# Kernel tuning notes

Measured on AMD Instinct MI355X. Metric: run time of the kernel, lower is better.

## Reference

```python
import jax, jax.numpy as jnp
import numpy as np

N = 40000          # nodes per type (dev, repo)
H, D = 8, 64       # heads, head dim
HID = H * D        # 512 hidden channels
OUT = 256
N_CONVS = 4        # 2 towers (res, link) x 2 layers
EDGE_TYPES = [(0, 1), (1, 0), (0, 0)]  # (src_type, dst_type)
SQRT_D = float(np.sqrt(D))


def _lin(x, w, b):
    return x @ w + b


def _seg_softmax(a, idx, n):
    m = jax.ops.segment_max(a, idx, num_segments=n)
    e = jnp.exp(a - m[idx])
    s = jax.ops.segment_sum(e, idx, num_segments=n)
    return e / (s[idx] + 1e-16)


def _hgt_conv(xs, edges, kw, kb, qw, qb, vw, vb, aw, ab, skip, a_rel, m_rel, p_rel):
    # xs: [x_dev, x_repo] each [N, HID]; edges: list of [2, E]
    k = [_lin(xs[t], kw[t], kb[t]).reshape(-1, H, D) for t in range(2)]
    q = [_lin(xs[t], qw[t], qb[t]).reshape(-1, H, D) for t in range(2)]
    v = [_lin(xs[t], vw[t], vb[t]).reshape(-1, H, D) for t in range(2)]
    out = [jnp.zeros_like(k[0]), jnp.zeros_like(k[1])]
    for r, (st, dt) in enumerate(EDGE_TYPES):
        src, dst = edges[r][0], edges[r][1]
        k_rel = jnp.einsum('nhd,hde->nhe', k[st], a_rel[r])
        v_rel = jnp.einsum('nhd,hde->nhe', v[st], m_rel[r])
        alpha = (q[dt][dst] * k_rel[src]).sum(-1) * p_rel[r] / SQRT_D  # [E, H]
        alpha = _seg_softmax(alpha, dst, N)
        msg = v_rel[src] * alpha[..., None]                            # [E, H, D]
        out[dt] = out[dt] + jax.ops.segment_sum(msg, dst, num_segments=N)
    res = []
    for t in range(2):
        o = _lin(jax.nn.gelu(out[t].reshape(-1, HID), approximate=False), aw[t], ab[t])
        g = jax.nn.sigmoid(skip[t])
        res.append(g * o + (1.0 - g) * xs[t])
    return res


def setup_inputs() -> dict:
    key = jax.random.key(0)
    ks = iter(jax.random.split(key, 48))
    def nrm(shape, scale=1.0):
        return jax.random.normal(next(ks), shape, dtype=jnp.float32) * scale
    E1, E2, E3, EP = 250000, 250000, 150000, 100000
    inp = {}
    inp['x_dev'] = nrm((N, HID))
    inp['x_repo'] = nrm((N, HID))
    inp['ei_dr'] = jax.random.randint(next(ks), (2, E1), 0, N, dtype=jnp.int32)
    inp['ei_rd'] = jax.random.randint(next(ks), (2, E2), 0, N, dtype=jnp.int32)
    inp['ei_dd'] = jax.random.randint(next(ks), (2, E3), 0, N, dtype=jnp.int32)
    inp['pos_edge'] = jax.random.randint(next(ks), (2, EP), 0, N, dtype=jnp.int32)
    inp['neg_edge'] = jax.random.randint(next(ks), (2, EP), 0, N, dtype=jnp.int32)
    s = 1.0 / np.sqrt(HID)
    for nm in ('k', 'q', 'v', 'a'):
        inp[nm + '_w'] = nrm((N_CONVS, 2, HID, HID), s)
        inp[nm + '_b'] = jnp.zeros((N_CONVS, 2, HID), jnp.float32)
    inp['skip'] = jnp.ones((N_CONVS, 2), jnp.float32)
    sd = 1.0 / np.sqrt(D)
    inp['a_rel'] = nrm((N_CONVS, 3, H, D, D), sd)
    inp['m_rel'] = nrm((N_CONVS, 3, H, D, D), sd)
    inp['p_rel'] = jnp.ones((N_CONVS, 3, H), jnp.float32)
    inp['reg_w1'] = nrm((HID, OUT), s); inp['reg_b1'] = jnp.zeros((OUT,), jnp.float32)
    inp['reg_w2'] = nrm((OUT, 1), 1.0 / np.sqrt(OUT)); inp['reg_b2'] = jnp.zeros((1,), jnp.float32)
    inp['src_w'] = nrm((HID, OUT), s); inp['src_b'] = jnp.zeros((OUT,), jnp.float32)
    inp['dst_w'] = nrm((HID, OUT), s); inp['dst_b'] = jnp.zeros((OUT,), jnp.float32)
    inp['fin_w'] = nrm((OUT, 1), 1.0 / np.sqrt(OUT)); inp['fin_b'] = jnp.zeros((1,), jnp.float32)
    return inp


def reference(x_dev, x_repo, ei_dr, ei_rd, ei_dd, pos_edge, neg_edge,
              k_w, k_b, q_w, q_b, v_w, v_b, a_w, a_b, skip,
              a_rel, m_rel, p_rel,
              reg_w1, reg_b1, reg_w2, reg_b2,
              src_w, src_b, dst_w, dst_b, fin_w, fin_b):
    edges = [ei_dr, ei_rd, ei_dd]

    def embed(conv_ids):
        xs = [x_dev, x_repo]
        for c in conv_ids:
            xs = _hgt_conv(xs, edges, k_w[c], k_b[c], q_w[c], q_b[c], v_w[c], v_b[c],
                           a_w[c], a_b[c], skip[c], a_rel[c], m_rel[c], p_rel[c])
            xs = [jax.nn.leaky_relu(x, 0.01) for x in xs]
        return xs

    res = embed([0, 1])   # embedding_res tower
    lnk = embed([2, 3])   # embedding_link tower
    emb_dev = res[0] + lnk[0]
    emb_repo = res[1] + lnk[1]

    fit_dev = _lin(_lin(emb_dev, reg_w1, reg_b1), reg_w2, reg_b2).squeeze(-1)
    fit_repo = _lin(_lin(emb_repo, reg_w1, reg_b1), reg_w2, reg_b2).squeeze(-1)

    def link(zs, zd):
        h = _lin(zs, src_w, src_b) * _lin(zd, dst_w, dst_b)
        return jax.nn.sigmoid(_lin(h, fin_w, fin_b)).squeeze(-1)

    pos = link(emb_dev[pos_edge[0]], emb_repo[pos_edge[1]])
    neg = link(emb_dev[neg_edge[0]], emb_repo[neg_edge[1]])
    score = jnp.concatenate([pos, neg], axis=0)
    return (fit_dev, fit_repo, score)
```

## Files before the change

kernel.cpp:

```cpp
#include <hip/hip_runtime.h>
#include <math.h>

#define NNODES 40000
#define NB ((size_t)20480000)
#define RPS 40004

typedef __attribute__((ext_vector_type(8))) short bf16x8;
typedef __attribute__((ext_vector_type(4))) float f32x4;

__device__ __forceinline__ ushort f2bf(float f) {
  unsigned u = __float_as_uint(f);
  u += 0x7FFFu + ((u >> 16) & 1u);
  return (ushort)(u >> 16);
}
__device__ __forceinline__ float b2f(ushort h) {
  return __uint_as_float((unsigned)h << 16);
}
__device__ __forceinline__ float gelu_f(float x) {
  return 0.5f * x * (1.0f + erff(x * 0.70710678118654752440f));
}

__device__ __forceinline__ void gll16(const ushort* g, ushort* l) {
  __builtin_amdgcn_global_load_lds(
      (const __attribute__((address_space(1))) unsigned int*)(const void*)g,
      (__attribute__((address_space(3))) unsigned int*)(void*)l, 16, 0, 0);
}

template<int EPI>
__global__ __launch_bounds__(256)
void gemm_bf16_kernel(const ushort* __restrict__ Av, const ushort* __restrict__ Bt,
                      const float* __restrict__ bias,
                      ushort* __restrict__ C0, ushort* __restrict__ C1,
                      int M, int PW, int RS,
                      const ushort* __restrict__ xprev, const float* __restrict__ skipv,
                      int nwgx)
{
  const int K = 512;
  __shared__ char smem[32768];
  ushort* Sm = (ushort*)smem;
  float*  Es = (float*)smem;

  const int nwg = (int)gridDim.x;
  const int q8 = nwg >> 3, r8 = nwg & 7;
  const int xcd = (int)blockIdx.x & 7, i8 = (int)blockIdx.x >> 3;
  const int logical = (xcd < r8 ? xcd * (q8 + 1) : r8 * (q8 + 1) + (xcd - r8) * q8) + i8;
  const int bm = (logical / nwgx) * 128;
  const int bnl = (logical % nwgx) * 128;
  const int pan = (bnl >= PW) ? 1 : 0;
  const int bn = bnl - pan * PW;
  ushort* __restrict__ C = pan ? C1 : C0;

  const int tid = threadIdx.x, lane = tid & 63, wave = tid >> 6;
  const int wr = (wave >> 1) * 64, wc = (wave & 1) * 64;
  const int fr = lane & 15, fq = lane >> 4;
  f32x4 acc[4][4] = {};

  const int rdsw = (fq ^ ((fr >> 1) & 3)) * 8;
  const int csrc = ((lane & 3) ^ ((lane >> 3) & 3)) * 8;
  const int r0 = wave * 32 + (lane >> 2);
  int ra0 = bm + r0;      if (ra0 >= M) ra0 = M - 1;
  int ra1 = bm + r0 + 16; if (ra1 >= M) ra1 = M - 1;
  const ushort* ga0 = Av + (size_t)ra0 * K + csrc;
  const ushort* ga1 = Av + (size_t)ra1 * K + csrc;
  const ushort* gb0 = Bt + (size_t)(bnl + r0) * K + csrc;
  const ushort* gb1 = Bt + (size_t)(bnl + r0 + 16) * K + csrc;
  ushort* la0[2] = {Sm + wave * 1024,        Sm + 8192 + wave * 1024};
  ushort* la1[2] = {la0[0] + 512,            la0[1] + 512};
  ushort* lb0[2] = {Sm + 4096 + wave * 1024, Sm + 12288 + wave * 1024};
  ushort* lb1[2] = {lb0[0] + 512,            lb0[1] + 512};

  gll16(ga0, la0[0]); gll16(ga1, la1[0]); gll16(gb0, lb0[0]); gll16(gb1, lb1[0]);
  ga0 += 32; ga1 += 32; gb0 += 32; gb1 += 32;
  gll16(ga0, la0[1]); gll16(ga1, la1[1]); gll16(gb0, lb0[1]); gll16(gb1, lb1[1]);
  ga0 += 32; ga1 += 32; gb0 += 32; gb1 += 32;

  #pragma unroll
  for (int it = 0; it < 16; ++it) {
    const int cur = it & 1;
    if (it < 15) asm volatile("s_waitcnt vmcnt(4)" ::: "memory");
    else         asm volatile("s_waitcnt vmcnt(0)" ::: "memory");
    __builtin_amdgcn_s_barrier();
    const ushort* Ab = Sm + cur * 8192;
    const ushort* Bb = Ab + 4096;
    bf16x8 af[4], bfv[4];
    #pragma unroll
    for (int i = 0; i < 4; ++i) {
      af[i]  = *(const bf16x8*)&Ab[(wr + i * 16 + fr) * 32 + rdsw];
      bfv[i] = *(const bf16x8*)&Bb[(wc + i * 16 + fr) * 32 + rdsw];
    }
    asm volatile("s_waitcnt lgkmcnt(0)" ::: "memory");
    __builtin_amdgcn_s_barrier();
    if (it < 14) {
      gll16(ga0, la0[cur]); gll16(ga1, la1[cur]); gll16(gb0, lb0[cur]); gll16(gb1, lb1[cur]);
      ga0 += 32; ga1 += 32; gb0 += 32; gb1 += 32;
    }
    #pragma unroll
    for (int mi = 0; mi < 4; ++mi)
      #pragma unroll
      for (int ni = 0; ni < 4; ++ni)
        acc[mi][ni] = __builtin_amdgcn_mfma_f32_16x16x32_bf16(af[mi], bfv[ni], acc[mi][ni], 0, 0, 0);
  }
  __syncthreads();

  float gate = 0.f, og = 0.f;
  if (EPI == 2) { gate = 1.f / (1.f + __expf(-skipv[0])); og = 1.f - gate; }
  #pragma unroll
  for (int qr = 0; qr < 4; ++qr) {
    __syncthreads();
    #pragma unroll
    for (int mi = 0; mi < 4; ++mi) {
      if (((wr + mi * 16) >> 5) != qr) continue;
      const int lr = ((wr + mi * 16) & 31) + fq * 4;
      #pragma unroll
      for (int ni = 0; ni < 4; ++ni) {
        const int col = wc + ni * 16 + fr;
        #pragma unroll
        for (int r = 0; r < 4; ++r)
          Es[(lr + r) * 132 + col] = acc[mi][ni][r];
      }
    }
    __syncthreads();
    const int lrow = tid >> 3;
    const int c0 = (tid & 7) * 16;
    const int grow = bm + qr * 32 + lrow;
    if (grow < M) {
      float v[16];
      #pragma unroll
      for (int j = 0; j < 4; ++j)
        *(float4*)&v[j * 4] = *(const float4*)&Es[lrow * 132 + c0 + j * 4];
      if (EPI == 1 || EPI == 2) {
        #pragma unroll
        for (int j = 0; j < 4; ++j) {
          float4 b4 = *(const float4*)(bias + bnl + c0 + j * 4);
          v[j*4] += b4.x; v[j*4+1] += b4.y; v[j*4+2] += b4.z; v[j*4+3] += b4.w;
        }
      }
      size_t base = (size_t)grow * RS + bn + c0;
      if (EPI == 2) {
        uint4 x0 = *(const uint4*)(xprev + base);
        uint4 x1 = *(const uint4*)(xprev + base + 8);
        #pragma unroll
        for (int j = 0; j < 8; ++j) {
          unsigned w = (j < 4) ? ((const unsigned*)&x0)[j] : ((const unsigned*)&x1)[j - 4];
          float a  = gate * v[2*j]   + og * __uint_as_float(w << 16);
          float bq = gate * v[2*j+1] + og * __uint_as_float(w & 0xFFFF0000u);
          v[2*j]   = a  > 0.f ? a  : 0.01f * a;
          v[2*j+1] = bq > 0.f ? bq : 0.01f * bq;
        }
      }
      if (EPI == 4) {
        uint4 x0 = *(const uint4*)(C + base);
        uint4 x1 = *(const uint4*)(C + base + 8);
        #pragma unroll
        for (int j = 0; j < 8; ++j) {
          unsigned w = (j < 4) ? ((const unsigned*)&x0)[j] : ((const unsigned*)&x1)[j - 4];
          v[2*j]   += __uint_as_float(w << 16);
          v[2*j+1] += __uint_as_float(w & 0xFFFF0000u);
        }
      }
      ushort ob[16];
      #pragma unroll
      for (int j = 0; j < 16; ++j) ob[j] = f2bf(v[j]);
      *(uint4*)(C + base)     = *(uint4*)&ob[0];
      *(uint4*)(C + base + 8) = *(uint4*)&ob[8];
    }
  }
}

__global__ __launch_bounds__(256)
void transpose_w_batch(const float* __restrict__ q_w, const float* __restrict__ a_w,
                       const float* __restrict__ src_w, const float* __restrict__ dst_w,
                       ushort* __restrict__ wqT, ushort* __restrict__ waT,
                       ushort* __restrict__ srcwT, ushort* __restrict__ dstwT)
{
  const int z = blockIdx.z;
  const float* W; ushort* Wt; int N;
  if (z < 8)       { W = q_w + (size_t)z * 262144;       Wt = wqT + (size_t)z * 262144;       N = 512; }
  else if (z < 16) { W = a_w + (size_t)(z - 8) * 262144; Wt = waT + (size_t)(z - 8) * 262144; N = 512; }
  else if (z == 16){ W = src_w; Wt = srcwT; N = 256; }
  else             { W = dst_w; Wt = dstwT; N = 256; }
  int bn = blockIdx.x * 32, bk = blockIdx.y * 32;
  if (bn >= N) return;
  __shared__ float t[32][33];
  int x = threadIdx.x & 31, y = threadIdx.x >> 5;
  #pragma unroll
  for (int yy = y; yy < 32; yy += 8) t[yy][x] = W[(size_t)(bk + yy) * N + bn + x];
  __syncthreads();
  #pragma unroll
  for (int yy = y; yy < 32; yy += 8) Wt[(size_t)(bn + yy) * 512 + bk + x] = f2bf(t[x][yy]);
}

__global__ __launch_bounds__(256)
void fold_rel_batch(const float* __restrict__ k_w, const float* __restrict__ k_b,
                    const float* __restrict__ v_w, const float* __restrict__ v_b,
                    const float* __restrict__ a_rel, const float* __restrict__ m_rel,
                    ushort* __restrict__ wkvT, float* __restrict__ bfuse)
{
  const int z = blockIdx.z;
  const int kv = z / 12, i = z % 12;
  const int c = i / 3, r = i % 3;
  const int st_tab[3] = {0, 1, 0};
  const int stp = st_tab[r];
  const float* Win  = (kv ? v_w : k_w) + (size_t)(c * 2 + stp) * 262144;
  const float* bin  = (kv ? v_b : k_b) + (size_t)(c * 2 + stp) * 512;
  const float* Arel = (kv ? m_rel : a_rel) + (size_t)i * 32768;
  const int h = blockIdx.x, kc = blockIdx.y;
  ushort* W2t = wkvT + (size_t)i * 524288 + (size_t)(h >> 2) * 262144
              + (size_t)(kv * 256 + (h & 3) * 64) * 512;
  float*  b2  = bfuse + i * 1024 + (h >> 2) * 512 + kv * 256 + (h & 3) * 64;

  __shared__ float Wl[64][65];
  __shared__ float Al[4096];
  for (int j = threadIdx.x; j < 4096; j += 256) Al[j] = Arel[(size_t)h * 4096 + j];
  {
    const int kk = threadIdx.x >> 2, d0 = (threadIdx.x & 3) * 16;
    const float* src = Win + (size_t)(kc * 64 + kk) * 512 + h * 64 + d0;
    #pragma unroll
    for (int j = 0; j < 4; ++j)
      *(float4*)&Wl[kk][d0 + j * 4] = *(const float4*)(src + j * 4);
  }
  __syncthreads();
  const int wave = threadIdx.x >> 6, lane = threadIdx.x & 63;
  #pragma unroll 4
  for (int rr = 0; rr < 16; ++rr) {
    const int e = wave * 16 + rr;
    float acc = 0.f;
    #pragma unroll
    for (int d = 0; d < 64; ++d) acc = fmaf(Wl[lane][d], Al[d * 64 + e], acc);
    W2t[(size_t)e * 512 + kc * 64 + lane] = f2bf(acc);
  }
  if (kc == 0 && wave == 0) {
    float acc = 0.f;
    #pragma unroll
    for (int d = 0; d < 64; ++d) acc = fmaf(bin[h * 64 + d], Al[d * 64 + lane], acc);
    b2[lane] = acc;
  }
}

__global__ __launch_bounds__(256)
void make_wfit_kernel(const float* __restrict__ w1, const float* __restrict__ b1,
                      const float* __restrict__ w2, const float* __restrict__ b2,
                      float* __restrict__ wfit)
{
  for (int k = threadIdx.x; k < 512; k += 256) {
    float acc = 0.f;
    for (int j = 0; j < 256; ++j) acc = fmaf(w1[(size_t)k * 256 + j], w2[j], acc);
    wfit[k] = acc;
  }
  if (threadIdx.x == 0) {
    float acc = 0.f;
    for (int j = 0; j < 256; ++j) acc = fmaf(b1[j], w2[j], acc);
    wfit[512] = acc + b2[0];
  }
}

__global__ __launch_bounds__(256)
void hist_batch(const int* __restrict__ d0, const int* __restrict__ d1,
                const int* __restrict__ d2, unsigned* __restrict__ cnt3)
{
  const int z = blockIdx.z;
  const int* dst = (z == 0) ? d0 : (z == 1) ? d1 : d2;
  const int E = (z == 2) ? 150000 : 250000;
  unsigned* cnt = cnt3 + (size_t)z * NNODES;
  for (int i = blockIdx.x * 256 + threadIdx.x; i < E; i += gridDim.x * 256)
    atomicAdd(&cnt[dst[i]], 1u);
}

__global__ __launch_bounds__(256)
void scan_batch(const unsigned* __restrict__ cnt3, unsigned* __restrict__ rowptr3,
                unsigned* __restrict__ woff3)
{
  const int z = blockIdx.x;
  const unsigned* cnt = cnt3 + (size_t)z * NNODES;
  unsigned* rowptr = rowptr3 + (size_t)z * RPS;
  unsigned* woff   = woff3 + (size_t)z * NNODES;
  __shared__ unsigned csum[256];
  const int t = threadIdx.x;
  const int lo = t * 160, hi = (lo + 160 < NNODES) ? lo + 160 : NNODES;
  unsigned s = 0;
  for (int i = lo; i < hi; i += 4) {
    uint4 v = *(const uint4*)&cnt[i];
    s += v.x + v.y + v.z + v.w;
  }
  csum[t] = s;
  __syncthreads();
  if (t == 0) {
    unsigned run = 0;
    for (int j = 0; j < 256; ++j) { unsigned v = csum[j]; csum[j] = run; run += v; }
    rowptr[NNODES] = run;
  }
  __syncthreads();
  unsigned run = csum[t];
  for (int i = lo; i < hi; i += 4) {
    uint4 cv = *(const uint4*)&cnt[i];
    uint4 rp;
    rp.x = run; run += cv.x;
    rp.y = run; run += cv.y;
    rp.z = run; run += cv.z;
    rp.w = run; run += cv.w;
    *(uint4*)&rowptr[i] = rp;
    *(uint4*)&woff[i]   = rp;
  }
}

__global__ __launch_bounds__(256)
void fill_batch(const int* __restrict__ e0, const int* __restrict__ e1,
                const int* __restrict__ e2, unsigned* __restrict__ woff3,
                unsigned* __restrict__ srcord)
{
  const int z = blockIdx.z;
  const int* e = (z == 0) ? e0 : (z == 1) ? e1 : e2;
  const int E = (z == 2) ? 150000 : 250000;
  const int* src = e;
  const int* dst = e + E;
  unsigned* woff = woff3 + (size_t)z * NNODES;
  unsigned* ord  = srcord + ((z == 0) ? 0 : (z == 1) ? 250000 : 500000);
  for (int i = blockIdx.x * 256 + threadIdx.x; i < E; i += gridDim.x * 256) {
    unsigned slot = atomicAdd(&woff[dst[i]], 1u);
    ord[slot] = (unsigned)src[i];
  }
}

template<int ACCUM, int GELU>
__global__ __launch_bounds__(256)
void fused_edge_kernel(const ushort* __restrict__ q, const ushort* __restrict__ KVh,
                      const unsigned* __restrict__ rowptr, const unsigned* __restrict__ srcord,
                      const float* __restrict__ prel, int hs,
                      const ushort* __restrict__ accin, ushort* __restrict__ outp)
{
  int d = (int)((blockIdx.x * 256u + threadIdx.x) >> 6);
  int lane = threadIdx.x & 63;
  if (d >= NNODES) return;
  unsigned start = rowptr[d], end = rowptr[d + 1];
  const int hl = lane >> 4;
  const int off = hl * 64 + (lane & 15) * 4;
  const float pscale = prel[hs * 4 + hl] * 0.125f;
  const size_t obase = (size_t)d * 512 + hs * 256 + off;

  uint2 qv = *(const uint2*)(q + obase);
  float qf0 = __uint_as_float(qv.x << 16),         qf1 = __uint_as_float(qv.x & 0xFFFF0000u);
  float qf2 = __uint_as_float(qv.y << 16),         qf3 = __uint_as_float(qv.y & 0xFFFF0000u);

  float m = -3e38f, ssum = 0.f;
  float a0 = 0.f, a1 = 0.f, a2 = 0.f, a3 = 0.f;
  if (start < end) {
    int sn = (int)srcord[start];
    const ushort* r0 = KVh + (size_t)sn * 512 + off;
    uint2 kv_c = *(const uint2*)r0;
    uint2 vv_c = *(const uint2*)(r0 + 256);
    const unsigned last = end - 1;
    for (unsigned idx = start; idx < end; ++idx) {
      unsigned idxn = (idx < last) ? idx + 1 : last;
      int sn2 = (int)srcord[idxn];
      const ushort* rn = KVh + (size_t)sn2 * 512 + off;
      uint2 kv_n = *(const uint2*)rn;
      uint2 vv_n = *(const uint2*)(rn + 256);
      float dot =      qf0 * __uint_as_float(kv_c.x << 16);
      dot = fmaf(qf1, __uint_as_float(kv_c.x & 0xFFFF0000u), dot);
      dot = fmaf(qf2, __uint_as_float(kv_c.y << 16),         dot);
      dot = fmaf(qf3, __uint_as_float(kv_c.y & 0xFFFF0000u), dot);
      dot += __shfl_xor(dot, 1);
      dot += __shfl_xor(dot, 2);
      dot += __shfl_xor(dot, 4);
      dot += __shfl_xor(dot, 8);
      float a = dot * pscale;
      if (a > m) {
        float r = __expf(m - a);
        ssum *= r; a0 *= r; a1 *= r; a2 *= r; a3 *= r;
        m = a;
      }
      float w = __expf(a - m);
      ssum += w;
      a0 = fmaf(w, __uint_as_float(vv_c.x << 16),         a0);
      a1 = fmaf(w, __uint_as_float(vv_c.x & 0xFFFF0000u), a1);
      a2 = fmaf(w, __uint_as_float(vv_c.y << 16),         a2);
      a3 = fmaf(w, __uint_as_float(vv_c.y & 0xFFFF0000u), a3);
      kv_c = kv_n; vv_c = vv_n;
    }
  }
  float rs = 1.f / (ssum + 1e-16f);
  float o0 = a0 * rs, o1 = a1 * rs, o2 = a2 * rs, o3 = a3 * rs;
  if (ACCUM) {
    uint2 old = *(const uint2*)(accin + obase);
    o0 += __uint_as_float(old.x << 16);  o1 += __uint_as_float(old.x & 0xFFFF0000u);
    o2 += __uint_as_float(old.y << 16);  o3 += __uint_as_float(old.y & 0xFFFF0000u);
  }
  if (GELU) { o0 = gelu_f(o0); o1 = gelu_f(o1); o2 = gelu_f(o2); o3 = gelu_f(o3); }
  uint2 ov;
  ov.x = (unsigned)f2bf(o0) | ((unsigned)f2bf(o1) << 16);
  ov.y = (unsigned)f2bf(o2) | ((unsigned)f2bf(o3) << 16);
  *(uint2*)(outp + obase) = ov;
}

template<int MODE>
__global__ __launch_bounds__(256)
void fitdot_kernel(const ushort* __restrict__ cur, const float* __restrict__ wfit,
                   float* __restrict__ out, int M)
{
  int row = (int)((blockIdx.x * 256u + threadIdx.x) >> 6);
  int lane = threadIdx.x & 63;
  if (row >= M) return;
  uint4 v = *(const uint4*)(cur + (size_t)row * 512 + lane * 8);
  const unsigned* pv = (const unsigned*)&v;
  float wreg[8];
  *(float4*)wreg       = *(const float4*)(wfit + lane * 8);
  *(float4*)(wreg + 4) = *(const float4*)(wfit + lane * 8 + 4);
  float acc = 0.f;
  #pragma unroll
  for (int j = 0; j < 4; ++j) {
    acc = fmaf(__uint_as_float(pv[j] << 16),         wreg[2 * j],     acc);
    acc = fmaf(__uint_as_float(pv[j] & 0xFFFF0000u), wreg[2 * j + 1], acc);
  }
  #pragma unroll
  for (int off = 1; off < 64; off <<= 1) acc += __shfl_xor(acc, off);
  if (lane == 0) {
    if (MODE == 0) out[row] = acc;
    else           out[row] += acc + wfit[512];
  }
}

__global__ __launch_bounds__(256)
void link_score_kernel(const ushort* __restrict__ se, const ushort* __restrict__ de,
                       const float* __restrict__ sb, const float* __restrict__ db,
                       const int* __restrict__ si, const int* __restrict__ di,
                       int E, const float* __restrict__ fw, const float* __restrict__ fb,
                       float* __restrict__ out)
{
  int wv = (int)((blockIdx.x * 256u + threadIdx.x) >> 6);
  int lane = threadIdx.x & 63;
  if (wv >= E) return;
  int s = si[wv], d = di[wv];
  ushort4 a = *(const ushort4*)(se + (size_t)s * 256 + lane * 4);
  ushort4 b = *(const ushort4*)(de + (size_t)d * 256 + lane * 4);
  float4 s4 = *(const float4*)(sb + lane * 4);
  float4 d4 = *(const float4*)(db + lane * 4);
  float4 w4 = *(const float4*)(fw + lane * 4);
  float acc = (b2f(a.x) + s4.x) * (b2f(b.x) + d4.x) * w4.x
            + (b2f(a.y) + s4.y) * (b2f(b.y) + d4.y) * w4.y
            + (b2f(a.z) + s4.z) * (b2f(b.z) + d4.z) * w4.z
            + (b2f(a.w) + s4.w) * (b2f(b.w) + d4.w) * w4.w;
  #pragma unroll
  for (int off = 1; off < 64; off <<= 1) acc += __shfl_xor(acc, off);
  if (lane == 0) out[wv] = 1.f / (1.f + __expf(-(acc + fb[0])));
}

__global__ __launch_bounds__(256)
void f32_to_bf16_kernel(const float* __restrict__ in, ushort* __restrict__ out, int n4)
{
  for (int i = blockIdx.x * 256 + threadIdx.x; i < n4; i += gridDim.x * 256) {
    float4 v = ((const float4*)in)[i];
    ushort4 o; o.x = f2bf(v.x); o.y = f2bf(v.y); o.z = f2bf(v.z); o.w = f2bf(v.w);
    ((ushort4*)out)[i] = o;
  }
}

__global__ void diag_kernel(float* __restrict__ out, float v)
{
  if (threadIdx.x == 0 && blockIdx.x == 0) out[0] = v;
}

extern "C" void kernel_launch(void* const* d_in, const int* in_sizes, int n_in,
                              void* d_out, int out_size, void* d_ws, size_t ws_size,
                              hipStream_t stream)
{
  const float* x_dev  = (const float*)d_in[0];
  const float* x_repo = (const float*)d_in[1];
  const int* ei[3] = {(const int*)d_in[2], (const int*)d_in[3], (const int*)d_in[4]};
  const int  Ecnt[3] = {250000, 250000, 150000};
  const int* pos_e = (const int*)d_in[5];
  const int* neg_e = (const int*)d_in[6];
  const float* k_w = (const float*)d_in[7];  const float* k_b = (const float*)d_in[8];
  const float* q_w = (const float*)d_in[9];  const float* q_b = (const float*)d_in[10];
  const float* v_w = (const float*)d_in[11]; const float* v_b = (const float*)d_in[12];
  const float* a_w = (const float*)d_in[13]; const float* a_b = (const float*)d_in[14];
  const float* skip  = (const float*)d_in[15];
  const float* a_rel = (const float*)d_in[16];
  const float* m_rel = (const float*)d_in[17];
  const float* p_rel = (const float*)d_in[18];
  const float* reg_w1 = (const float*)d_in[19]; const float* reg_b1 = (const float*)d_in[20];
  const float* reg_w2 = (const float*)d_in[21]; const float* reg_b2 = (const float*)d_in[22];
  const float* src_w  = (const float*)d_in[23]; const float* src_b  = (const float*)d_in[24];
  const float* dst_w  = (const float*)d_in[25]; const float* dst_b  = (const float*)d_in[26];
  const float* fin_w  = (const float*)d_in[27]; const float* fin_b  = (const float*)d_in[28];
  float* out = (float*)d_out;

  const size_t SE = (size_t)NNODES * 256;
  ushort* st   = (ushort*)d_ws;
  ushort* cur0 = st;
  ushort* cur1 = st + NB;
  ushort* S1   = st + 2 * NB;
  ushort* S2   = st + 3 * NB;
  ushort* KVh  = st + 4 * NB;
  ushort* se   = st + 5 * NB;
  ushort* de   = se + SE;
  ushort* wqT   = de + SE;
  ushort* waT   = wqT + (size_t)8 * 262144;
  ushort* wkvT  = waT + (size_t)8 * 262144;
  ushort* srcwT = wkvT + (size_t)12 * 524288;
  ushort* dstwT = srcwT + 131072;
  float*  bfuse = (float*)(dstwT + 131072);
  float*  wfit  = bfuse + 12288;
  unsigned* rowptr3 = (unsigned*)(wfit + 516);
  unsigned* srcord  = rowptr3 + (size_t)3 * RPS;
  unsigned* cnt3    = srcord + 650000;
  unsigned* woff3   = cnt3 + (size_t)3 * NNODES;
  const size_t need = (size_t)((char*)(woff3 + (size_t)3 * NNODES) - (char*)d_ws);
  if (ws_size < need) {
    diag_kernel<<<1, 64, 0, stream>>>(out, 1000.0f + (float)(ws_size / 1000000));
    return;
  }
  const size_t ord_off[3] = {0, 250000, 500000};

  transpose_w_batch<<<dim3(16, 16, 18), 256, 0, stream>>>(q_w, a_w, src_w, dst_w,
                                                          wqT, waT, srcwT, dstwT);
  fold_rel_batch<<<dim3(8, 8, 24), 256, 0, stream>>>(k_w, k_b, v_w, v_b, a_rel, m_rel,
                                                     wkvT, bfuse);
  make_wfit_kernel<<<1, 256, 0, stream>>>(reg_w1, reg_b1, reg_w2, reg_b2, wfit);
  hipMemsetAsync(cnt3, 0, (size_t)3 * NNODES * 4, stream);
  hist_batch<<<dim3(977, 1, 3), 256, 0, stream>>>(ei[0] + Ecnt[0], ei[1] + Ecnt[1],
                                                  ei[2] + Ecnt[2], cnt3);
  scan_batch<<<3, 256, 0, stream>>>(cnt3, rowptr3, woff3);
  fill_batch<<<dim3(977, 1, 3), 256, 0, stream>>>(ei[0], ei[1], ei[2], woff3, srcord);

  auto gemmQ = [&](const ushort* A, int t, ushort* C) {
    gemm_bf16_kernel<1><<<1252, 256, 0, stream>>>(A, wqT + (size_t)t * 262144,
        q_b + (size_t)t * 512, C, C, NNODES, 512, 512, nullptr, nullptr, 4);
  };
  auto gemmKVh = [&](int i, int hs, const ushort* A) {
    gemm_bf16_kernel<1><<<1252, 256, 0, stream>>>(A,
        wkvT + (size_t)i * 524288 + (size_t)hs * 262144,
        bfuse + (size_t)i * 1024 + hs * 512,
        KVh, KVh + 256, NNODES, 256, 512, nullptr, nullptr, 4);
  };
  auto gemmA = [&](int t, const ushort* Abuf, ushort* curb) {
    gemm_bf16_kernel<2><<<1252, 256, 0, stream>>>(Abuf, waT + (size_t)t * 262144,
        a_b + (size_t)t * 512, curb, curb, NNODES, 512, 512, curb, skip + t, 4);
  };

  auto run_conv = [&](int c) {
    const int t0 = 2 * c, t1 = 2 * c + 1;
    const int i0 = 3 * c, i1 = 3 * c + 1, i2 = 3 * c + 2;
    gemmQ(cur0, t0, S1);
    for (int hs = 0; hs < 2; ++hs) {
      gemmKVh(i1, hs, cur1);
      fused_edge_kernel<0, 0><<<10000, 256, 0, stream>>>(S1, KVh,
          rowptr3 + RPS, srcord + ord_off[1], p_rel + (size_t)i1 * 8, hs, nullptr, S2);
    }
    for (int hs = 0; hs < 2; ++hs) {
      gemmKVh(i2, hs, cur0);
      fused_edge_kernel<1, 1><<<10000, 256, 0, stream>>>(S1, KVh,
          rowptr3 + 2 * RPS, srcord + ord_off[2], p_rel + (size_t)i2 * 8, hs, S2, S2);
    }
    gemmQ(cur1, t1, S1);
    for (int hs = 0; hs < 2; ++hs) {
      gemmKVh(i0, hs, cur0);
      fused_edge_kernel<0, 1><<<10000, 256, 0, stream>>>(S1, KVh,
          rowptr3, srcord + ord_off[0], p_rel + (size_t)i0 * 8, hs, nullptr, S1);
    }
    gemmA(t0, S2, cur0);
    gemmA(t1, S1, cur1);
  };

  f32_to_bf16_kernel<<<2048, 256, 0, stream>>>(x_dev,  cur0, (int)(NB / 4));
  f32_to_bf16_kernel<<<2048, 256, 0, stream>>>(x_repo, cur1, (int)(NB / 4));
  run_conv(0);
  run_conv(1);
  fitdot_kernel<0><<<10000, 256, 0, stream>>>(cur0, wfit, out, NNODES);
  fitdot_kernel<0><<<10000, 256, 0, stream>>>(cur1, wfit, out + NNODES, NNODES);
  gemm_bf16_kernel<3><<<626, 256, 0, stream>>>(cur0, srcwT, nullptr, se, se, NNODES, 256, 256, nullptr, nullptr, 2);
  gemm_bf16_kernel<3><<<626, 256, 0, stream>>>(cur1, dstwT, nullptr, de, de, NNODES, 256, 256, nullptr, nullptr, 2);

  f32_to_bf16_kernel<<<2048, 256, 0, stream>>>(x_dev,  cur0, (int)(NB / 4));
  f32_to_bf16_kernel<<<2048, 256, 0, stream>>>(x_repo, cur1, (int)(NB / 4));
  run_conv(2);
  run_conv(3);
  fitdot_kernel<1><<<10000, 256, 0, stream>>>(cur0, wfit, out, NNODES);
  fitdot_kernel<1><<<10000, 256, 0, stream>>>(cur1, wfit, out + NNODES, NNODES);
  gemm_bf16_kernel<4><<<626, 256, 0, stream>>>(cur0, srcwT, nullptr, se, se, NNODES, 256, 256, nullptr, nullptr, 2);
  gemm_bf16_kernel<4><<<626, 256, 0, stream>>>(cur1, dstwT, nullptr, de, de, NNODES, 256, 256, nullptr, nullptr, 2);

  link_score_kernel<<<25000, 256, 0, stream>>>(se, de, src_b, dst_b, pos_e, pos_e + 100000,
                                               100000, fin_w, fin_b, out + 80000);
  link_score_kernel<<<25000, 256, 0, stream>>>(se, de, src_b, dst_b, neg_e, neg_e + 100000,
                                               100000, fin_w, fin_b, out + 180000);
}
```

Before: 2.900 ms.

## Process all heads in one edge pass with full-width KV GEMM and 16-bit indices

Adds a path where one GEMM produces K and V for all 8 heads (N=1024) into a double-width buffer. A new edge kernel then walks each destination's CSR neighbour list once, with each lane handling 8 channels through 16-byte gathers. This replaces the two half-head GEMM plus edge-kernel passes, so rowptr and srcord are read and the neighbour loop runs half as often. Source indices in srcord are stored as ushort, which fits the 40000 nodes and halves index traffic. The full path needs an extra node-sized buffer and is chosen only when the workspace is large enough; otherwise the old half path runs.

Result: faster. 2.669 ms (-8.0%).

```diff
diff --git a/kernel.cpp b/kernel.cpp
--- a/kernel.cpp
+++ b/kernel.cpp
@@ -306,7 +306,7 @@
 __global__ __launch_bounds__(256)
 void fill_batch(const int* __restrict__ e0, const int* __restrict__ e1,
                 const int* __restrict__ e2, unsigned* __restrict__ woff3,
-                unsigned* __restrict__ srcord)
+                ushort* __restrict__ srcord)
 {
   const int z = blockIdx.z;
   const int* e = (z == 0) ? e0 : (z == 1) ? e1 : e2;
@@ -314,17 +314,17 @@
   const int* src = e;
   const int* dst = e + E;
   unsigned* woff = woff3 + (size_t)z * NNODES;
-  unsigned* ord  = srcord + ((z == 0) ? 0 : (z == 1) ? 250000 : 500000);
+  ushort* ord = srcord + ((z == 0) ? 0 : (z == 1) ? 250000 : 500000);
   for (int i = blockIdx.x * 256 + threadIdx.x; i < E; i += gridDim.x * 256) {
     unsigned slot = atomicAdd(&woff[dst[i]], 1u);
-    ord[slot] = (unsigned)src[i];
+    ord[slot] = (ushort)src[i];
   }
 }
 
 template<int ACCUM, int GELU>
 __global__ __launch_bounds__(256)
 void fused_edge_kernel(const ushort* __restrict__ q, const ushort* __restrict__ KVh,
-                      const unsigned* __restrict__ rowptr, const unsigned* __restrict__ srcord,
+                      const unsigned* __restrict__ rowptr, const ushort* __restrict__ srcord,
                       const float* __restrict__ prel, int hs,
                       const ushort* __restrict__ accin, ushort* __restrict__ outp)
 {
@@ -392,6 +392,97 @@
   *(uint2*)(outp + obase) = ov;
 }
 
+template<int ACCUM, int GELU>
+__global__ __launch_bounds__(256)
+void fused_edge_full_kernel(const ushort* __restrict__ q, const ushort* __restrict__ KVf,
+                            const unsigned* __restrict__ rowptr, const ushort* __restrict__ srcord,
+                            const float* __restrict__ prel,
+                            const ushort* __restrict__ accin, ushort* __restrict__ outp)
+{
+  int d = (int)((blockIdx.x * 256u + threadIdx.x) >> 6);
+  int lane = threadIdx.x & 63;
+  if (d >= NNODES) return;
+  unsigned start = rowptr[d], end = rowptr[d + 1];
+  const int h = lane >> 3, sub = lane & 7;
+  const int koff = (h >> 2) * 512 + (h & 3) * 64 + sub * 8;
+  const float pscale = prel[h] * 0.125f;
+  const size_t obase = (size_t)d * 512 + h * 64 + sub * 8;
+
+  uint4 qv = *(const uint4*)(q + obase);
+  const unsigned* pq = (const unsigned*)&qv;
+  float qf[8];
+  #pragma unroll
+  for (int j = 0; j < 4; ++j) {
+    qf[2*j]   = __uint_as_float(pq[j] << 16);
+    qf[2*j+1] = __uint_as_float(pq[j] & 0xFFFF0000u);
+  }
+
+  float m = -3e38f, ssum = 0.f;
+  float av[8] = {};
+  if (start < end) {
+    int sn = (int)srcord[start];
+    const ushort* r0 = KVf + (size_t)sn * 1024 + koff;
+    uint4 kv_c = *(const uint4*)r0;
+    uint4 vv_c = *(const uint4*)(r0 + 256);
+    const unsigned last = end - 1;
+    for (unsigned idx = start; idx < end; ++idx) {
+      unsigned idxn = (idx < last) ? idx + 1 : last;
+      int sn2 = (int)srcord[idxn];
+      const ushort* rn = KVf + (size_t)sn2 * 1024 + koff;
+      uint4 kv_n = *(const uint4*)rn;
+      uint4 vv_n = *(const uint4*)(rn + 256);
+      const unsigned* pk = (const unsigned*)&kv_c;
+      float dot = 0.f;
+      #pragma unroll
+      for (int j = 0; j < 4; ++j) {
+        dot = fmaf(qf[2*j],   __uint_as_float(pk[j] << 16),         dot);
+        dot = fmaf(qf[2*j+1], __uint_as_float(pk[j] & 0xFFFF0000u), dot);
+      }
+      dot += __shfl_xor(dot, 1);
+      dot += __shfl_xor(dot, 2);
+      dot += __shfl_xor(dot, 4);
+      float a = dot * pscale;
+      if (a > m) {
+        float r = __expf(m - a);
+        ssum *= r;
+        #pragma unroll
+        for (int j = 0; j < 8; ++j) av[j] *= r;
+        m = a;
+      }
+      float w = __expf(a - m);
+      ssum += w;
+      const unsigned* pv = (const unsigned*)&vv_c;
+      #pragma unroll
+      for (int j = 0; j < 4; ++j) {
+        av[2*j]   = fmaf(w, __uint_as_float(pv[j] << 16),         av[2*j]);
+        av[2*j+1] = fmaf(w, __uint_as_float(pv[j] & 0xFFFF0000u), av[2*j+1]);
+      }
+      kv_c = kv_n; vv_c = vv_n;
+    }
+  }
+  float rs = 1.f / (ssum + 1e-16f);
+  float o[8];
+  #pragma unroll
+  for (int j = 0; j < 8; ++j) o[j] = av[j] * rs;
+  if (ACCUM) {
+    uint4 old = *(const uint4*)(accin + obase);
+    const unsigned* po = (const unsigned*)&old;
+    #pragma unroll
+    for (int j = 0; j < 4; ++j) {
+      o[2*j]   += __uint_as_float(po[j] << 16);
+      o[2*j+1] += __uint_as_float(po[j] & 0xFFFF0000u);
+    }
+  }
+  if (GELU) {
+    #pragma unroll
+    for (int j = 0; j < 8; ++j) o[j] = gelu_f(o[j]);
+  }
+  ushort ob[8];
+  #pragma unroll
+  for (int j = 0; j < 8; ++j) ob[j] = f2bf(o[j]);
+  *(uint4*)(outp + obase) = *(uint4*)ob;
+}
+
 template<int MODE>
 __global__ __launch_bounds__(256)
 void fitdot_kernel(const ushort* __restrict__ cur, const float* __restrict__ wfit,
@@ -485,13 +576,32 @@
   float* out = (float*)d_out;
 
   const size_t SE = (size_t)NNODES * 256;
+  const size_t tail_bytes =
+      (size_t)8 * 262144 * 2
+    + (size_t)8 * 262144 * 2
+    + (size_t)12 * 524288 * 2
+    + 131072ull * 2 * 2
+    + 12288ull * 4 + 516ull * 4
+    + (size_t)3 * RPS * 4
+    + 650000ull * 2 + 4
+    + (size_t)3 * NNODES * 4 * 2;
+  const size_t need_full = (6 * NB + 2 * SE) * 2 + tail_bytes;
+  const size_t need_half = (5 * NB + 2 * SE) * 2 + tail_bytes;
+  int FULL;
+  if      (ws_size >= need_full) FULL = 1;
+  else if (ws_size >= need_half) FULL = 0;
+  else {
+    diag_kernel<<<1, 64, 0, stream>>>(out, 1000.0f + (float)(ws_size / 1000000));
+    return;
+  }
+
   ushort* st   = (ushort*)d_ws;
   ushort* cur0 = st;
   ushort* cur1 = st + NB;
   ushort* S1   = st + 2 * NB;
   ushort* S2   = st + 3 * NB;
-  ushort* KVh  = st + 4 * NB;
-  ushort* se   = st + 5 * NB;
+  ushort* KV   = st + 4 * NB;
+  ushort* se   = st + (FULL ? 6 : 5) * NB;
   ushort* de   = se + SE;
   ushort* wqT   = de + SE;
   ushort* waT   = wqT + (size_t)8 * 262144;
@@ -501,14 +611,9 @@
   float*  bfuse = (float*)(dstwT + 131072);
   float*  wfit  = bfuse + 12288;
   unsigned* rowptr3 = (unsigned*)(wfit + 516);
-  unsigned* srcord  = rowptr3 + (size_t)3 * RPS;
-  unsigned* cnt3    = srcord + 650000;
+  ushort*   srcord  = (ushort*)(rowptr3 + (size_t)3 * RPS);
+  unsigned* cnt3    = (unsigned*)(srcord + 650000 + 2);
   unsigned* woff3   = cnt3 + (size_t)3 * NNODES;
-  const size_t need = (size_t)((char*)(woff3 + (size_t)3 * NNODES) - (char*)d_ws);
-  if (ws_size < need) {
-    diag_kernel<<<1, 64, 0, stream>>>(out, 1000.0f + (float)(ws_size / 1000000));
-    return;
-  }
   const size_t ord_off[3] = {0, 250000, 500000};
 
   transpose_w_batch<<<dim3(16, 16, 18), 256, 0, stream>>>(q_w, a_w, src_w, dst_w,
@@ -530,7 +635,11 @@
     gemm_bf16_kernel<1><<<1252, 256, 0, stream>>>(A,
         wkvT + (size_t)i * 524288 + (size_t)hs * 262144,
         bfuse + (size_t)i * 1024 + hs * 512,
-        KVh, KVh + 256, NNODES, 256, 512, nullptr, nullptr, 4);
+        KV, KV + 256, NNODES, 256, 512, nullptr, nullptr, 4);
+  };
+  auto gemmKVf = [&](int i, const ushort* A) {
+    gemm_bf16_kernel<1><<<2504, 256, 0, stream>>>(A, wkvT + (size_t)i * 524288,
+        bfuse + (size_t)i * 1024, KV, KV, NNODES, 1024, 1024, nullptr, nullptr, 8);
   };
   auto gemmA = [&](int t, const ushort* Abuf, ushort* curb) {
     gemm_bf16_kernel<2><<<1252, 256, 0, stream>>>(Abuf, waT + (size_t)t * 262144,
@@ -541,21 +650,34 @@
     const int t0 = 2 * c, t1 = 2 * c + 1;
     const int i0 = 3 * c, i1 = 3 * c + 1, i2 = 3 * c + 2;
     gemmQ(cur0, t0, S1);
-    for (int hs = 0; hs < 2; ++hs) {
-      gemmKVh(i1, hs, cur1);
-      fused_edge_kernel<0, 0><<<10000, 256, 0, stream>>>(S1, KVh,
-          rowptr3 + RPS, srcord + ord_off[1], p_rel + (size_t)i1 * 8, hs, nullptr, S2);
-    }
-    for (int hs = 0; hs < 2; ++hs) {
-      gemmKVh(i2, hs, cur0);
-      fused_edge_kernel<1, 1><<<10000, 256, 0, stream>>>(S1, KVh,
-          rowptr3 + 2 * RPS, srcord + ord_off[2], p_rel + (size_t)i2 * 8, hs, S2, S2);
-    }
-    gemmQ(cur1, t1, S1);
-    for (int hs = 0; hs < 2; ++hs) {
-      gemmKVh(i0, hs, cur0);
-      fused_edge_kernel<0, 1><<<10000, 256, 0, stream>>>(S1, KVh,
-          rowptr3, srcord + ord_off[0], p_rel + (size_t)i0 * 8, hs, nullptr, S1);
+    if (FULL) {
+      gemmKVf(i1, cur1);
+      fused_edge_full_kernel<0, 0><<<10000, 256, 0, stream>>>(S1, KV,
+          rowptr3 + RPS, srcord + ord_off[1], p_rel + (size_t)i1 * 8, nullptr, S2);
+      gemmKVf(i2, cur0);
+      fused_edge_full_kernel<1, 1><<<10000, 256, 0, stream>>>(S1, KV,
+          rowptr3 + 2 * RPS, srcord + ord_off[2], p_rel + (size_t)i2 * 8, S2, S2);
+      gemmKVf(i0, cur0);
+      gemmQ(cur1, t1, S1);
+      fused_edge_full_kernel<0, 1><<<10000, 256, 0, stream>>>(S1, KV,
+          rowptr3, srcord + ord_off[0], p_rel + (size_t)i0 * 8, nullptr, S1);
+    } else {
+      for (int hs = 0; hs < 2; ++hs) {
+        gemmKVh(i1, hs, cur1);
+        fused_edge_kernel<0, 0><<<10000, 256, 0, stream>>>(S1, KV,
+            rowptr3 + RPS, srcord + ord_off[1], p_rel + (size_t)i1 * 8, hs, nullptr, S2);
+      }
+      for (int hs = 0; hs < 2; ++hs) {
+        gemmKVh(i2, hs, cur0);
+        fused_edge_kernel<1, 1><<<10000, 256, 0, stream>>>(S1, KV,
+            rowptr3 + 2 * RPS, srcord + ord_off[2], p_rel + (size_t)i2 * 8, hs, S2, S2);
+      }
+      gemmQ(cur1, t1, S1);
+      for (int hs = 0; hs < 2; ++hs) {
+        gemmKVh(i0, hs, cur0);
+        fused_edge_kernel<0, 1><<<10000, 256, 0, stream>>>(S1, KV,
+            rowptr3, srcord + ord_off[0], p_rel + (size_t)i0 * 8, hs, nullptr, S1);
+      }
     }
     gemmA(t0, S2, cur0);
     gemmA(t1, S1, cur1);
```
